# Performance work log

Hardware: AMD Instinct MI355X
Metric: run time of the kernel (lower is better)

Reference implementation:

```python
import jax, jax.numpy as jnp
import numpy as np

DIM = 384

def setup_inputs() -> dict:
    key = jax.random.key(0)
    k1, k2, k3 = jax.random.split(key, 3)
    x = jax.random.normal(k1, (8, DIM, 56, 56), dtype=jnp.float32)
    # nn.Linear(dim, dim, bias=False): weight shape [out, in]; y = x @ W^T
    w1 = jax.random.normal(k2, (DIM, DIM), dtype=jnp.float32) * (1.0 / np.sqrt(DIM))
    w2 = jax.random.normal(k3, (DIM, DIM), dtype=jnp.float32) * (1.0 / np.sqrt(DIM))
    return {"x": x, "w1": w1, "w2": w2}

def reference(x, w1, w2):
    B, C, H, W = x.shape
    scale = C ** (-0.5)
    t = x.reshape(B, C, H * W).transpose(0, 2, 1)  # [B, N, C]
    q = jnp.einsum('bnc,dc->bnd', t, w1)           # linear1(x)
    attn = jnp.einsum('bnd,bmd->bnm', q, t) * scale  # QK^T scaled
    attn = jax.nn.softmax(attn, axis=-1)
    v = jnp.einsum('bnc,dc->bnd', t, w2)           # linear2(x)
    out = jnp.einsum('bnm,bmd->bnd', attn, v)      # [B, N, C]
    return out.transpose(0, 2, 1).reshape(B, C, H, W)
```

## Files before the change

kernel.cpp:

```cpp
#include <hip/hip_runtime.h>
#include <hip/hip_bf16.h>

#define DIM 384
#define SEQ 3136
#define NBATCH 8

typedef __attribute__((ext_vector_type(8))) short short8;
typedef __attribute__((ext_vector_type(4))) float fx4;
typedef __attribute__((ext_vector_type(4))) int i4;
typedef __hip_bfloat16 bf16;

#define MFMA(a,b,c) __builtin_amdgcn_mfma_f32_16x16x32_bf16(a,b,c,0,0,0)

__global__ __launch_bounds__(256) void ktransw(const float* __restrict__ x,
                                               bf16* __restrict__ kb,
                                               const float* __restrict__ w1,
                                               const float* __restrict__ w2,
                                               bf16* __restrict__ w1b,
                                               bf16* __restrict__ w2b) {
  if (blockIdx.z == 8) {
    int id = blockIdx.y * 49 + blockIdx.x;
    int i0 = id * 512 + threadIdx.x;
    if (i0 < DIM * DIM) { w1b[i0] = __float2bfloat16(w1[i0]); w2b[i0] = __float2bfloat16(w2[i0]); }
    int i1 = i0 + 256;
    if (i1 < DIM * DIM) { w1b[i1] = __float2bfloat16(w1[i1]); w2b[i1] = __float2bfloat16(w2[i1]); }
    return;
  }
  __shared__ float t[64][65];
  int b = blockIdx.z;
  int n0 = blockIdx.x * 64, c0 = blockIdx.y * 64;
  int tid = threadIdx.x;
  {
    int nl = tid & 63, cl = tid >> 6;
    const float* xp = x + ((size_t)b * DIM + c0) * SEQ + n0;
    #pragma unroll
    for (int p = 0; p < 16; ++p) {
      int c = cl * 16 + p;
      t[c][nl] = xp[(size_t)c * SEQ + nl];
    }
  }
  __syncthreads();
  {
    int cp = (tid & 31) * 2, nr = tid >> 5;
    bf16* kp = kb + ((size_t)b * SEQ + n0) * DIM + c0;
    #pragma unroll
    for (int p = 0; p < 8; ++p) {
      int n = nr * 8 + p;
      __hip_bfloat162 v;
      v.x = __float2bfloat16(t[cp][n]);
      v.y = __float2bfloat16(t[cp + 1][n]);
      *reinterpret_cast<__hip_bfloat162*>(&kp[(size_t)n * DIM + cp]) = v;
    }
  }
}

__global__ __launch_bounds__(256, 3) void kgemm2(const bf16* __restrict__ Kb,
                                                 const bf16* __restrict__ w1b,
                                                 const bf16* __restrict__ w2b,
                                                 bf16* __restrict__ Qb,
                                                 bf16* __restrict__ Vt) {
  __shared__ __align__(16) bf16 At[64][200];
  __shared__ __align__(16) bf16 Bs[64][200];
  int z = blockIdx.z, id = blockIdx.x;
  const bf16 *A, *Bt;
  bf16* out;
  long long Abs, Bbs, Obs;
  int ldo, bx, by, b;
  if (z < 8) {
    b = z; A = Kb; Abs = (long long)SEQ * DIM; Bt = w1b; Bbs = 0;
    out = Qb; Obs = (long long)SEQ * DIM; ldo = DIM;
    bx = id % 49; by = id / 49;
  } else {
    b = z - 8; A = w2b; Abs = 0; Bt = Kb; Bbs = (long long)SEQ * DIM;
    out = Vt; Obs = (long long)DIM * SEQ; ldo = SEQ;
    bx = id % 6; by = id / 6;
  }
  int tid = threadIdx.x;
  const bf16* Ab = A + (size_t)b * Abs + (size_t)bx * 64 * DIM;
  const bf16* Bb = Bt + (size_t)b * Bbs + (size_t)by * 64 * DIM;
  int row = tid >> 2, cb = (tid & 3) * 48;
  int wave = tid >> 6, lane = tid & 63;
  int r = lane & 15, kq = lane >> 4;
  fx4 zero = {0.f, 0.f, 0.f, 0.f};
  fx4 acc[4];
  #pragma unroll
  for (int i = 0; i < 4; ++i) acc[i] = zero;
  #pragma unroll
  for (int kb2 = 0; kb2 < DIM; kb2 += 192) {
    if (kb2) __syncthreads();
    {
      const i4* ga = (const i4*)(Ab + (size_t)row * DIM + kb2 + cb);
      const i4* gb = (const i4*)(Bb + (size_t)row * DIM + kb2 + cb);
      i4* la = (i4*)(&At[row][cb]);
      i4* lb = (i4*)(&Bs[row][cb]);
      #pragma unroll
      for (int p = 0; p < 6; ++p) { la[p] = ga[p]; lb[p] = gb[p]; }
    }
    __syncthreads();
    __builtin_amdgcn_s_setprio(1);
    #pragma unroll
    for (int ks = 0; ks < 6; ++ks) {
      short8 af = *(const short8*)(&At[wave * 16 + r][ks * 32 + kq * 8]);
      #pragma unroll
      for (int ct = 0; ct < 4; ++ct) {
        short8 bfr = *(const short8*)(&Bs[ct * 16 + r][ks * 32 + kq * 8]);
        acc[ct] = MFMA(af, bfr, acc[ct]);
      }
    }
    __builtin_amdgcn_s_setprio(0);
  }
  bf16* ob = out + (size_t)b * Obs
           + (size_t)(bx * 64 + wave * 16 + kq * 4) * ldo + by * 64;
  #pragma unroll
  for (int ct = 0; ct < 4; ++ct)
    #pragma unroll
    for (int rr = 0; rr < 4; ++rr)
      ob[(size_t)rr * ldo + ct * 16 + r] = __float2bfloat16(acc[ct][rr]);
}

__global__ __launch_bounds__(256, 2) void kattn(const bf16* __restrict__ Qb,
                                                const bf16* __restrict__ Kb,
                                                const bf16* __restrict__ Vt,
                                                float* __restrict__ out) {
  __shared__ __align__(16) bf16 Kl[64][DIM + 8];
  __shared__ __align__(16) bf16 Pl[4][16][68];
  __shared__ float rsum[64];

  int b = blockIdx.x;
  int n0 = blockIdx.y * 64;
  int tid = threadIdx.x;
  int wave = tid >> 6, lane = tid & 63;
  int r = lane & 15, kq = lane >> 4;

  short8 qf[12];
  {
    const bf16* qp = Qb + ((size_t)b * SEQ + n0 + wave * 16 + r) * DIM + kq * 8;
    #pragma unroll
    for (int ks = 0; ks < 12; ++ks) qf[ks] = *(const short8*)(qp + ks * 32);
  }
  fx4 zero = {0.f, 0.f, 0.f, 0.f};
  fx4 acc[4][6];
  #pragma unroll
  for (int i = 0; i < 4; ++i)
    #pragma unroll
    for (int j = 0; j < 6; ++j) acc[i][j] = zero;
  float rs[4] = {0.f, 0.f, 0.f, 0.f};
  const float cexp = 0.07362223f;

  const bf16* kbase = Kb + (size_t)b * SEQ * DIM;
  const bf16* vbase = Vt + (size_t)b * DIM * SEQ;

  int srow = tid >> 2, scb = (tid & 3) * 96;

  for (int im = 0; im < SEQ / 64; ++im) {
    int m0 = im * 64;
    {
      const i4* g = (const i4*)(kbase + (size_t)(m0 + srow) * DIM + scb);
      i4* l = (i4*)(&Kl[srow][scb]);
      #pragma unroll
      for (int p = 0; p < 12; ++p) l[p] = g[p];
    }
    __syncthreads();
    short8 vf[2][6];
    #pragma unroll
    for (int ks2 = 0; ks2 < 2; ++ks2)
      #pragma unroll
      for (int dtl = 0; dtl < 6; ++dtl) {
        int d = (wave * 6 + dtl) * 16 + r;
        vf[ks2][dtl] = *(const short8*)(vbase + (size_t)d * SEQ + m0 + ks2 * 32 + kq * 8);
      }
    fx4 sa[4];
    #pragma unroll
    for (int ct = 0; ct < 4; ++ct) sa[ct] = zero;
    __builtin_amdgcn_s_setprio(1);
    #pragma unroll
    for (int ks = 0; ks < 12; ++ks) {
      #pragma unroll
      for (int ct = 0; ct < 4; ++ct) {
        short8 bfr = *(const short8*)(&Kl[ct * 16 + r][ks * 32 + kq * 8]);
        sa[ct] = MFMA(qf[ks], bfr, sa[ct]);
      }
    }
    __builtin_amdgcn_s_setprio(0);
    #pragma unroll
    for (int rr = 0; rr < 4; ++rr) {
      float e0 = exp2f(sa[0][rr] * cexp);
      float e1 = exp2f(sa[1][rr] * cexp);
      float e2 = exp2f(sa[2][rr] * cexp);
      float e3 = exp2f(sa[3][rr] * cexp);
      int row = kq * 4 + rr;
      Pl[wave][row][r]      = __float2bfloat16(e0);
      Pl[wave][row][16 + r] = __float2bfloat16(e1);
      Pl[wave][row][32 + r] = __float2bfloat16(e2);
      Pl[wave][row][48 + r] = __float2bfloat16(e3);
      rs[rr] += (e0 + e1) + (e2 + e3);
    }
    __syncthreads();
    __builtin_amdgcn_s_setprio(1);
    #pragma unroll
    for (int ks2 = 0; ks2 < 2; ++ks2) {
      short8 pa[4];
      #pragma unroll
      for (int rg = 0; rg < 4; ++rg)
        pa[rg] = *(const short8*)(&Pl[rg][r][ks2 * 32 + kq * 8]);
      #pragma unroll
      for (int dtl = 0; dtl < 6; ++dtl) {
        #pragma unroll
        for (int rg = 0; rg < 4; ++rg)
          acc[rg][dtl] = MFMA(pa[rg], vf[ks2][dtl], acc[rg][dtl]);
      }
    }
    __builtin_amdgcn_s_setprio(0);
  }
  #pragma unroll
  for (int rr = 0; rr < 4; ++rr) {
    float v = rs[rr];
    v += __shfl_xor(v, 1);
    v += __shfl_xor(v, 2);
    v += __shfl_xor(v, 4);
    v += __shfl_xor(v, 8);
    if (r == 0) rsum[wave * 16 + kq * 4 + rr] = v;
  }
  __syncthreads();
  float* ob = out + (size_t)b * DIM * SEQ;
  #pragma unroll
  for (int rg = 0; rg < 4; ++rg) {
    #pragma unroll
    for (int rr = 0; rr < 4; ++rr) {
      float inv = 1.0f / rsum[rg * 16 + kq * 4 + rr];
      int n = n0 + rg * 16 + kq * 4 + rr;
      #pragma unroll
      for (int dtl = 0; dtl < 6; ++dtl) {
        int d = (wave * 6 + dtl) * 16 + r;
        ob[(size_t)d * SEQ + n] = acc[rg][dtl][rr] * inv;
      }
    }
  }
}

extern "C" void kernel_launch(void* const* d_in, const int* in_sizes, int n_in,
                              void* d_out, int out_size, void* d_ws, size_t ws_size,
                              hipStream_t stream) {
  const float* x  = (const float*)d_in[0];
  const float* w1 = (const float*)d_in[1];
  const float* w2 = (const float*)d_in[2];
  float* out = (float*)d_out;

  char* ws = (char*)d_ws;
  size_t SZ = (size_t)NBATCH * SEQ * DIM * sizeof(bf16);
  bf16* Kb  = (bf16*)(ws);
  bf16* Qb  = (bf16*)(ws + SZ);
  bf16* Vt  = (bf16*)(ws + 2 * SZ);
  bf16* w1b = (bf16*)(ws + 3 * SZ);
  bf16* w2b = (bf16*)(ws + 3 * SZ + (size_t)DIM * DIM * sizeof(bf16));

  ktransw<<<dim3(SEQ / 64, DIM / 64, NBATCH + 1), 256, 0, stream>>>(
      x, Kb, w1, w2, w1b, w2b);
  kgemm2<<<dim3(294, 1, 2 * NBATCH), 256, 0, stream>>>(Kb, w1b, w2b, Qb, Vt);
  kattn<<<dim3(NBATCH, SEQ / 64), 256, 0, stream>>>(Qb, Kb, Vt, out);
}
```

Before: 298.7 us.

## Stage Q in LDS and stream K per wave; compute row sums via MFMA

Swaps operand residency in the attention kernel: the 64-row Q tile is now loaded once into shared memory, and each wave reads its 16 rows of K straight from global memory into registers on every iteration. This removes the per-iteration cooperative K copy into LDS. Softmax row sums now come from an extra MFMA of P against a vector of ones instead of per-lane adds and a shuffle reduction. In exchange, K is read from global memory by each wave with no LDS reuse, a second barrier is added per iteration, and the row sums are accumulated from bf16-rounded probabilities.

```diff
diff --git a/kernel.cpp b/kernel.cpp
--- a/kernel.cpp
+++ b/kernel.cpp
@@ -122,9 +122,8 @@
                                                 const bf16* __restrict__ Kb,
                                                 const bf16* __restrict__ Vt,
                                                 float* __restrict__ out) {
-  __shared__ __align__(16) bf16 Kl[64][DIM + 8];
+  __shared__ __align__(16) bf16 Ql[64][DIM + 8];
   __shared__ __align__(16) bf16 Pl[4][16][68];
-  __shared__ float rsum[64];
 
   int b = blockIdx.x;
   int n0 = blockIdx.y * 64;
@@ -132,35 +131,41 @@
   int wave = tid >> 6, lane = tid & 63;
   int r = lane & 15, kq = lane >> 4;
 
-  short8 qf[12];
   {
-    const bf16* qp = Qb + ((size_t)b * SEQ + n0 + wave * 16 + r) * DIM + kq * 8;
-    #pragma unroll
-    for (int ks = 0; ks < 12; ++ks) qf[ks] = *(const short8*)(qp + ks * 32);
-  }
+    int srow = tid >> 2, scb = (tid & 3) * 96;
+    const i4* g = (const i4*)(Qb + ((size_t)b * SEQ + n0 + srow) * DIM + scb);
+    i4* l = (i4*)(&Ql[srow][scb]);
+    #pragma unroll
+    for (int p = 0; p < 12; ++p) l[p] = g[p];
+  }
+
   fx4 zero = {0.f, 0.f, 0.f, 0.f};
   fx4 acc[4][6];
   #pragma unroll
   for (int i = 0; i < 4; ++i)
     #pragma unroll
     for (int j = 0; j < 6; ++j) acc[i][j] = zero;
-  float rs[4] = {0.f, 0.f, 0.f, 0.f};
+  fx4 accr[4];
+  #pragma unroll
+  for (int i = 0; i < 4; ++i) accr[i] = zero;
+  short8 ones;
+  #pragma unroll
+  for (int i = 0; i < 8; ++i) ones[i] = (short)0x3F80;
   const float cexp = 0.07362223f;
 
   const bf16* kbase = Kb + (size_t)b * SEQ * DIM;
   const bf16* vbase = Vt + (size_t)b * DIM * SEQ;
 
-  int srow = tid >> 2, scb = (tid & 3) * 96;
+  __syncthreads();
 
   for (int im = 0; im < SEQ / 64; ++im) {
     int m0 = im * 64;
+    short8 kf[12];
     {
-      const i4* g = (const i4*)(kbase + (size_t)(m0 + srow) * DIM + scb);
-      i4* l = (i4*)(&Kl[srow][scb]);
-      #pragma unroll
-      for (int p = 0; p < 12; ++p) l[p] = g[p];
-    }
-    __syncthreads();
+      const bf16* kp = kbase + (size_t)(m0 + wave * 16 + r) * DIM + kq * 8;
+      #pragma unroll
+      for (int ks = 0; ks < 12; ++ks) kf[ks] = *(const short8*)(kp + ks * 32);
+    }
     short8 vf[2][6];
     #pragma unroll
     for (int ks2 = 0; ks2 < 2; ++ks2)
@@ -177,24 +182,18 @@
     for (int ks = 0; ks < 12; ++ks) {
       #pragma unroll
       for (int ct = 0; ct < 4; ++ct) {
-        short8 bfr = *(const short8*)(&Kl[ct * 16 + r][ks * 32 + kq * 8]);
-        sa[ct] = MFMA(qf[ks], bfr, sa[ct]);
+        short8 qfr = *(const short8*)(&Ql[ct * 16 + r][ks * 32 + kq * 8]);
+        sa[ct] = MFMA(qfr, kf[ks], sa[ct]);
       }
     }
     __builtin_amdgcn_s_setprio(0);
     #pragma unroll
-    for (int rr = 0; rr < 4; ++rr) {
-      float e0 = exp2f(sa[0][rr] * cexp);
-      float e1 = exp2f(sa[1][rr] * cexp);
-      float e2 = exp2f(sa[2][rr] * cexp);
-      float e3 = exp2f(sa[3][rr] * cexp);
-      int row = kq * 4 + rr;
-      Pl[wave][row][r]      = __float2bfloat16(e0);
-      Pl[wave][row][16 + r] = __float2bfloat16(e1);
-      Pl[wave][row][32 + r] = __float2bfloat16(e2);
-      Pl[wave][row][48 + r] = __float2bfloat16(e3);
-      rs[rr] += (e0 + e1) + (e2 + e3);
-    }
+    for (int ct = 0; ct < 4; ++ct)
+      #pragma unroll
+      for (int rr = 0; rr < 4; ++rr) {
+        float e = exp2f(sa[ct][rr] * cexp);
+        Pl[ct][kq * 4 + rr][wave * 16 + r] = __float2bfloat16(e);
+      }
     __syncthreads();
     __builtin_amdgcn_s_setprio(1);
     #pragma unroll
@@ -203,6 +202,9 @@
       #pragma unroll
       for (int rg = 0; rg < 4; ++rg)
         pa[rg] = *(const short8*)(&Pl[rg][r][ks2 * 32 + kq * 8]);
+      #pragma unroll
+      for (int rg = 0; rg < 4; ++rg)
+        accr[rg] = MFMA(pa[rg], ones, accr[rg]);
       #pragma unroll
       for (int dtl = 0; dtl < 6; ++dtl) {
         #pragma unroll
@@ -211,23 +213,14 @@
       }
     }
     __builtin_amdgcn_s_setprio(0);
-  }
-  #pragma unroll
-  for (int rr = 0; rr < 4; ++rr) {
-    float v = rs[rr];
-    v += __shfl_xor(v, 1);
-    v += __shfl_xor(v, 2);
-    v += __shfl_xor(v, 4);
-    v += __shfl_xor(v, 8);
-    if (r == 0) rsum[wave * 16 + kq * 4 + rr] = v;
-  }
-  __syncthreads();
+    __syncthreads();
+  }
   float* ob = out + (size_t)b * DIM * SEQ;
   #pragma unroll
   for (int rg = 0; rg < 4; ++rg) {
     #pragma unroll
     for (int rr = 0; rr < 4; ++rr) {
-      float inv = 1.0f / rsum[rg * 16 + kq * 4 + rr];
+      float inv = 1.0f / accr[rg][rr];
       int n = n0 + rg * 16 + kq * 4 + rr;
       #pragma unroll
       for (int dtl = 0; dtl < 6; ++dtl) {
```

Measured after the change: 383.6 us. +28.4%, slower.
